# Performance work log

Hardware: AMD Instinct MI355X
Metric: run time of the kernel (lower is better)

Reference implementation:

```python
import jax, jax.numpy as jnp
import numpy as np

H, W = 32, 56
CK, CV = 64, 512
N = 16 * H * W  # long + work memory fully populated: 16 frames of H*W entries
TOP_K = 30


def setup_inputs() -> dict:
    key = jax.random.key(0)
    k1, k2, k3, k4, k5 = jax.random.split(key, 5)
    return {
        "q_key": jax.random.normal(k1, (1, CK, H, W), dtype=jnp.float32),
        "q_selection": jax.random.uniform(k2, (1, CK, H, W), dtype=jnp.float32),
        "mem_key": jax.random.normal(k3, (1, CK, N), dtype=jnp.float32),
        "mem_shrinkage": jax.random.uniform(k4, (1, N, 1), dtype=jnp.float32),
        "mem_value": jax.random.normal(k5, (2, CV, N), dtype=jnp.float32),
    }


def reference(q_key, q_selection, mem_key, mem_shrinkage, mem_value):
    b, ck, h, w = q_key.shape
    hw = h * w
    qk = q_key.reshape(1, ck, hw)          # [1, CK, HW]
    qs = q_selection.reshape(1, ck, hw)    # [1, CK, HW]

    mk = jnp.swapaxes(mem_key, 1, 2)       # [1, N, CK]
    # negative weighted squared L2 distance via matmul algebra
    a_sq = jnp.matmul(mk * mk, qs)                    # [1, N, HW]
    two_ab = 2.0 * jnp.matmul(mk, qk * qs)            # [1, N, HW]
    b_sq = jnp.sum(qs * qk * qk, axis=1, keepdims=True)  # [1, 1, HW]
    sim = (-a_sq + two_ab - b_sq) * mem_shrinkage / jnp.sqrt(jnp.float32(ck))  # [1, N, HW]

    # topk over the memory axis (dim=1), softmax over selected entries, scatter back
    simT = jnp.swapaxes(sim, 1, 2)                    # [1, HW, N]
    vals, idx = jax.lax.top_k(simT, TOP_K)            # [1, HW, K]
    x_exp = jnp.exp(vals)
    x_exp = x_exp / jnp.sum(x_exp, axis=-1, keepdims=True)
    i0 = jnp.arange(1)[:, None, None]
    i1 = jnp.arange(hw)[None, :, None]
    affT = jnp.zeros_like(simT).at[i0, i1, idx].set(x_exp)  # [1, HW, N]
    affinity = jnp.swapaxes(affT, 1, 2)               # [1, N, HW]

    out = jnp.matmul(mem_value, affinity)             # [2, CV, HW] (batch-broadcast)
    return out.reshape(2, CV, h, w)
```

## Files before the change

### kernel.cpp

```cpp
#include <hip/hip_runtime.h>
#include <math.h>

#define HW      1792
#define NMEM    28672
#define NCHUNK  3584
#define TOPK    30
#define CTARGET 64
#define BINS    4096
#define VCACHE  3072
#define SIMB    448
#define WPS     7

typedef __attribute__((ext_vector_type(8))) short bf16x8;
typedef __attribute__((ext_vector_type(8))) unsigned short u16x8;
typedef __attribute__((ext_vector_type(4))) float f32x4;
typedef __attribute__((ext_vector_type(4))) _Float16 h4;

static __device__ __forceinline__ unsigned short f2bf(float v) {
  unsigned b = __float_as_uint(v);
  return (unsigned short)((b + 0x7FFFu + ((b >> 16) & 1u)) >> 16);
}
static __device__ __forceinline__ float bf2f(unsigned short h) {
  return __uint_as_float(((unsigned)h) << 16);
}
static __device__ __forceinline__ unsigned fkey(float v) {
  return __float_as_uint(-v) & 0x7FFFFFFFu;
}
static __device__ __forceinline__ void gl_lds16(const void* g, void* l) {
  __builtin_amdgcn_global_load_lds(
      (const __attribute__((address_space(1))) unsigned*)g,
      (__attribute__((address_space(3))) unsigned*)l, 16, 0, 0);
}

__global__ __launch_bounds__(256)
void k_prep_b(const float* __restrict__ mk, const float* __restrict__ shr_in,
              unsigned short* __restrict__ Bh,
              float* __restrict__ mkT, float* __restrict__ shr_s)
{
  const int n = blockIdx.x * 256 + threadIdx.x;
  shr_s[n] = shr_in[n] * 0.125f;
  for (int cb = 0; cb < 64; cb += 8) {
    u16x8 h1, h2;
    float vv[8];
    #pragma unroll
    for (int j = 0; j < 8; ++j) {
      float v = mk[(size_t)(cb + j) * NMEM + n];
      vv[j] = v;
      h1[j] = f2bf(v);
      h2[j] = f2bf(v * v);
    }
    const int s = cb >> 3;
    *reinterpret_cast<u16x8*>(&Bh[((size_t)s * NMEM + n) * 8])       = h1;
    *reinterpret_cast<u16x8*>(&Bh[((size_t)(s + 8) * NMEM + n) * 8]) = h2;
    *reinterpret_cast<float4*>(&mkT[(size_t)n * 64 + cb])     = make_float4(vv[0], vv[1], vv[2], vv[3]);
    *reinterpret_cast<float4*>(&mkT[(size_t)n * 64 + cb + 4]) = make_float4(vv[4], vv[5], vv[6], vv[7]);
  }
}

__global__ __launch_bounds__(256)
void k_prep_u(const float* __restrict__ q_key, const float* __restrict__ q_sel,
              unsigned short* __restrict__ Uh, unsigned short* __restrict__ Ul,
              float* __restrict__ bsq)
{
  const int p = blockIdx.x * 256 + threadIdx.x;
  float bs = 0.f;
  for (int cb = 0; cb < 64; cb += 8) {
    u16x8 h1, l1, h2, l2;
    #pragma unroll
    for (int j = 0; j < 8; ++j) {
      int c = cb + j;
      float k = q_key[(size_t)c * HW + p];
      float s = q_sel[(size_t)c * HW + p];
      float u = 2.f * k * s;
      float w = -s;
      bs = fmaf(s * k, k, bs);
      unsigned short h = f2bf(u); h1[j] = h; l1[j] = f2bf(u - bf2f(h));
      unsigned short g = f2bf(w); h2[j] = g; l2[j] = f2bf(w - bf2f(g));
    }
    const int s = cb >> 3;
    *reinterpret_cast<u16x8*>(&Uh[((size_t)s * HW + p) * 8])       = h1;
    *reinterpret_cast<u16x8*>(&Ul[((size_t)s * HW + p) * 8])       = l1;
    *reinterpret_cast<u16x8*>(&Uh[((size_t)(s + 8) * HW + p) * 8]) = h2;
    *reinterpret_cast<u16x8*>(&Ul[((size_t)(s + 8) * HW + p) * 8]) = l2;
  }
  bsq[p] = bs;
}

__global__ __launch_bounds__(256, 2)
void k_sim(const unsigned short* __restrict__ Uh, const unsigned short* __restrict__ Ul,
           const unsigned short* __restrict__ Bh,
           const float* __restrict__ bsq, const float* __restrict__ shr_s,
           float* __restrict__ pmax)
{
  __shared__ char smem[65536] __attribute__((aligned(16)));
  const int tid = threadIdx.x;
  const int wid = tid >> 6, lane = tid & 63;
  const int lr = lane & 15, lg = lane >> 4;
  const int pb = blockIdx.x % 14, st = blockIdx.x / 14;
  const int pw = pb * 128 + wid * 32;
  const int w0 = st * WPS;

  bf16x8 a0h[4], a0l[4], a1h[4], a1l[4];
  #pragma unroll
  for (int t = 0; t < 4; ++t) {
    const size_t e0 = ((size_t)(t * 4 + lg) * HW + pw + lr) * 8;
    const size_t e1 = e0 + 16 * 8;
    a0h[t] = *reinterpret_cast<const bf16x8*>(&Uh[e0]);
    a0l[t] = *reinterpret_cast<const bf16x8*>(&Ul[e0]);
    a1h[t] = *reinterpret_cast<const bf16x8*>(&Uh[e1]);
    a1l[t] = *reinterpret_cast<const bf16x8*>(&Ul[e1]);
  }
  float bq[2][4];
  #pragma unroll
  for (int pt = 0; pt < 2; ++pt)
    #pragma unroll
    for (int r = 0; r < 4; ++r) bq[pt][r] = bsq[pw + pt * 16 + 4 * lg + r];

  auto stage = [&](int buf, int i) {
    const int n0 = (w0 + i) * 128;
    #pragma unroll
    for (int j = 0; j < 8; ++j) {
      const int idx = j * 256 + tid;
      const int s = idx >> 7, rr = idx & 127;
      gl_lds16((const char*)Bh + ((size_t)s * NMEM + n0 + rr) * 16,
               smem + buf * 32768 + idx * 16);
    }
  };

  stage(0, 0);
  int buf = 0;
  for (int i = 0; i < WPS; ++i) {
    __syncthreads();
    if (i + 1 < WPS) stage(buf ^ 1, i + 1);

    f32x4 acc[2][8];
    #pragma unroll
    for (int a = 0; a < 2; ++a)
      #pragma unroll
      for (int b = 0; b < 8; ++b) acc[a][b] = (f32x4){0.f, 0.f, 0.f, 0.f};

    const short* lb = (const short*)(smem + buf * 32768);
    #pragma unroll
    for (int t = 0; t < 4; ++t) {
      #pragma unroll
      for (int nt = 0; nt < 8; ++nt) {
        bf16x8 bh = *reinterpret_cast<const bf16x8*>(
            &lb[((t * 4 + lg) * 128 + nt * 16 + lr) * 8]);
        acc[0][nt] = __builtin_amdgcn_mfma_f32_16x16x32_bf16(a0h[t], bh, acc[0][nt], 0, 0, 0);
        acc[0][nt] = __builtin_amdgcn_mfma_f32_16x16x32_bf16(a0l[t], bh, acc[0][nt], 0, 0, 0);
        acc[1][nt] = __builtin_amdgcn_mfma_f32_16x16x32_bf16(a1h[t], bh, acc[1][nt], 0, 0, 0);
        acc[1][nt] = __builtin_amdgcn_mfma_f32_16x16x32_bf16(a1l[t], bh, acc[1][nt], 0, 0, 0);
      }
    }

    const int wgl = w0 + i;
    const int n0 = wgl * 128;
    float shv[8];
    #pragma unroll
    for (int nt = 0; nt < 8; ++nt) shv[nt] = shr_s[n0 + nt * 16 + lr];
    #pragma unroll
    for (int pt = 0; pt < 2; ++pt) {
      #pragma unroll
      for (int r = 0; r < 4; ++r) {
        float mx = -INFINITY;
        #pragma unroll
        for (int nt = 0; nt < 8; ++nt)
          mx = fmaxf(mx, (acc[pt][nt][r] - bq[pt][r]) * shv[nt]);
        pmax[(size_t)(pw + pt * 16 + 4 * lg + r) * NCHUNK + wgl * 16 + lr] = mx;
      }
    }
    buf ^= 1;
  }
}

__global__ __launch_bounds__(256)
void k_transpose_h(const float* __restrict__ mv, _Float16* __restrict__ mvT)
{
  __shared__ float t[64][65];
  const int n0 = blockIdx.x * 64, ch0 = blockIdx.y * 64;
  const int tid = threadIdx.x;
  for (int i = tid; i < 64 * 16; i += 256) {
    int r = i >> 4, c4 = (i & 15) << 2;
    float4 v = *reinterpret_cast<const float4*>(&mv[(size_t)(ch0 + r) * NMEM + n0 + c4]);
    t[r][c4] = v.x; t[r][c4 + 1] = v.y; t[r][c4 + 2] = v.z; t[r][c4 + 3] = v.w;
  }
  __syncthreads();
  for (int i = tid; i < 64 * 16; i += 256) {
    int r = i >> 4, c4 = (i & 15) << 2;
    h4 hv = {(_Float16)t[c4][r], (_Float16)t[c4 + 1][r],
             (_Float16)t[c4 + 2][r], (_Float16)t[c4 + 3][r]};
    *reinterpret_cast<h4*>(&mvT[(size_t)(n0 + r) * 1024 + ch0 + c4]) = hv;
  }
}

__device__ __forceinline__ void find_cross(int* hist, int* lsum, int* wsum,
                                           int tid, int target, int* sB, int* sNA)
{
  const int base = tid * (BINS / 256);
  int ls = 0;
  #pragma unroll
  for (int k = 0; k < BINS / 256; ++k) ls += hist[base + k];
  lsum[tid] = ls;
  __syncthreads();
  int lane = tid & 63, wv = tid >> 6;
  int v = ls;
  #pragma unroll
  for (int off = 1; off < 64; off <<= 1) {
    int t = __shfl_up(v, off);
    if (lane >= off) v += t;
  }
  if (lane == 63) wsum[wv] = v;
  __syncthreads();
  int wo = 0;
  for (int k = 0; k < wv; ++k) wo += wsum[k];
  int run = wo + v - ls;
  #pragma unroll 1
  for (int k = 0; k < BINS / 256; ++k) {
    int h = hist[base + k];
    if (run < target && run + h >= target) { *sB = base + k; *sNA = run; }
    run += h;
  }
  __syncthreads();
}

__global__ __launch_bounds__(256)
void k_select(const float* __restrict__ pmax, const float* __restrict__ mkT,
              const float* __restrict__ q_key, const float* __restrict__ q_sel,
              const float* __restrict__ shr_s,
              float* __restrict__ wgt, int* __restrict__ widx)
{
  __shared__ int            hist[BINS];
  __shared__ float          sqk[64], sqs[64];
  __shared__ unsigned short chl[NCHUNK];
  __shared__ float          vcache[VCACHE];
  __shared__ unsigned       au[96];
  __shared__ int            ai[96];
  __shared__ unsigned       bu[1024];
  __shared__ int            bi[1024];
  __shared__ float          fv[32];
  __shared__ int            fi[32];
  __shared__ float          ew[32];
  __shared__ int            lsum[256], wsum[4];
  __shared__ int            sB, sNA, cA, cB, sSC;
  __shared__ float          sSum;

  const int pix = blockIdx.x;
  const int tid = threadIdx.x;

  if (tid < 64) {
    sqk[tid] = q_key[(size_t)tid * HW + pix];
    sqs[tid] = q_sel[(size_t)tid * HW + pix];
  }
  for (int i = tid; i < BINS; i += 256) hist[i] = 0;
  if (tid == 0) { sSC = 0; cA = 0; cB = 0; }
  __syncthreads();

  float m[NCHUNK / 256];
  const float* pm = pmax + (size_t)pix * NCHUNK;
  #pragma unroll
  for (int j = 0; j < NCHUNK / 256; ++j) m[j] = pm[tid + 256 * j];
  #pragma unroll
  for (int j = 0; j < NCHUNK / 256; ++j) atomicAdd(&hist[fkey(m[j]) >> 19], 1);
  __syncthreads();
  find_cross(hist, lsum, wsum, tid, CTARGET, &sB, &sNA);
  {
    const int B = sB;
    #pragma unroll
    for (int j = 0; j < NCHUNK / 256; ++j)
      if ((int)(fkey(m[j]) >> 19) <= B) {
        int k = atomicAdd(&sSC, 1);
        chl[k] = (unsigned short)(tid + 256 * j);
      }
  }
  __syncthreads();
  const int SC = sSC, NC = SC * 8;
  for (int i = tid; i < BINS; i += 256) hist[i] = 0;
  __syncthreads();

  const float4* sqk4 = reinterpret_cast<const float4*>(sqk);
  const float4* sqs4 = reinterpret_cast<const float4*>(sqs);

  for (int c = tid; c < NC; c += 256) {
    const int cc = chl[c >> 3];
    const int n = ((cc >> 4) << 7) + (cc & 15) + ((c & 7) << 4);
    const float4* mr = reinterpret_cast<const float4*>(mkT + (size_t)n * 64);
    float s = 0.f;
    #pragma unroll
    for (int j = 0; j < 16; ++j) {
      float4 q = mr[j], k4 = sqk4[j], s4 = sqs4[j];
      float d0 = q.x - k4.x, d1 = q.y - k4.y, d2 = q.z - k4.z, d3 = q.w - k4.w;
      s = fmaf(s4.x * d0, d0, s); s = fmaf(s4.y * d1, d1, s);
      s = fmaf(s4.z * d2, d2, s); s = fmaf(s4.w * d3, d3, s);
    }
    float v = -s * shr_s[n];
    if (c < VCACHE) vcache[c] = v;
    atomicAdd(&hist[fkey(v) >> 19], 1);
  }
  __syncthreads();
  find_cross(hist, lsum, wsum, tid, TOPK, &sB, &sNA);

  {
    const int B2 = sB;
    for (int c = tid; c < NC; c += 256) {
      const int cc = chl[c >> 3];
      const int n = ((cc >> 4) << 7) + (cc & 15) + ((c & 7) << 4);
      float v;
      if (c < VCACHE) v = vcache[c];
      else {
        const float4* mr = reinterpret_cast<const float4*>(mkT + (size_t)n * 64);
        float s = 0.f;
        #pragma unroll
        for (int j = 0; j < 16; ++j) {
          float4 q = mr[j], k4 = sqk4[j], s4 = sqs4[j];
          float d0 = q.x - k4.x, d1 = q.y - k4.y, d2 = q.z - k4.z, d3 = q.w - k4.w;
          s = fmaf(s4.x * d0, d0, s); s = fmaf(s4.y * d1, d1, s);
          s = fmaf(s4.z * d2, d2, s); s = fmaf(s4.w * d3, d3, s);
        }
        v = -s * shr_s[n];
      }
      unsigned u = fkey(v);
      int bin = (int)(u >> 19);
      if (bin < B2)       { int k = atomicAdd(&cA, 1); au[k] = u; ai[k] = n; }
      else if (bin == B2) { int k = atomicAdd(&cB, 1); if (k < 1024) { bu[k] = u; bi[k] = n; } }
    }
  }
  __syncthreads();
  {
    const int nAv = cA, mm = (cB < 1024 ? cB : 1024), need = TOPK - nAv;
    for (int t = tid; t < mm; t += 256) {
      unsigned u = bu[t]; int id = bi[t];
      int r = 0;
      for (int k2 = 0; k2 < mm; ++k2) {
        unsigned uk = bu[k2];
        r += (uk < u) || (uk == u && bi[k2] < id);
      }
      if (r < need) { au[nAv + r] = u; ai[nAv + r] = id; }
    }
  }
  __syncthreads();

  if (tid < TOPK) {
    unsigned u = au[tid]; int id = ai[tid];
    int r = 0;
    for (int k2 = 0; k2 < TOPK; ++k2) {
      unsigned uk = au[k2];
      r += (uk < u) || (uk == u && ai[k2] < id);
    }
    fv[r] = -__uint_as_float(u); fi[r] = id;
  }
  __syncthreads();
  if (tid < 32) {
    float e = (tid < TOPK) ? expf(fv[tid]) : 0.f;
    if (tid < TOPK) ew[tid] = e;
    float ss = e;
    #pragma unroll
    for (int off = 16; off > 0; off >>= 1) ss += __shfl_down(ss, off);
    if (tid == 0) sSum = ss;
  }
  __syncthreads();
  if (tid < TOPK) {
    wgt [(size_t)pix * 32 + tid] = ew[tid] / sSum;
    widx[(size_t)pix * 32 + tid] = fi[tid];
  }
}

__global__ __launch_bounds__(256)
void k_gather_h(const _Float16* __restrict__ mvT, const float* __restrict__ wgt,
                const int* __restrict__ widx, float* __restrict__ out)
{
  __shared__ float sw[8][TOPK];
  __shared__ int   si[8][TOPK];
  __shared__ float sbuf[256][9];
  const int p0 = blockIdx.x * 8, chg = blockIdx.y * 256;
  const int tid = threadIdx.x;

  for (int i = tid; i < 8 * TOPK; i += 256) {
    int q = i / TOPK, k = i - q * TOPK;
    sw[q][k] = wgt [(size_t)(p0 + q) * 32 + k];
    si[q][k] = widx[(size_t)(p0 + q) * 32 + k];
  }
  __syncthreads();

  const int ch = chg + tid;
  #pragma unroll 2
  for (int q = 0; q < 8; ++q) {
    float a = 0.f;
    #pragma unroll
    for (int k = 0; k < TOPK; ++k)
      a = fmaf(sw[q][k], (float)mvT[(size_t)si[q][k] * 1024 + ch], a);
    sbuf[tid][q] = a;
  }
  __syncthreads();

  for (int i = tid; i < 256 * 8; i += 256) {
    int cl = i >> 3, q = i & 7;
    out[(size_t)(chg + cl) * HW + p0 + q] = sbuf[cl][q];
  }
}

__global__ __launch_bounds__(256)
void k_gather_f(const float* __restrict__ src, const float* __restrict__ wgt,
                const int* __restrict__ widx, float* __restrict__ out,
                long n_stride, long ch_stride)
{
  __shared__ float sw[8][TOPK];
  __shared__ int   si[8][TOPK];
  __shared__ float sbuf[256][9];
  const int p0 = blockIdx.x * 8, chg = blockIdx.y * 256;
  const int tid = threadIdx.x;

  for (int i = tid; i < 8 * TOPK; i += 256) {
    int q = i / TOPK, k = i - q * TOPK;
    sw[q][k] = wgt [(size_t)(p0 + q) * 32 + k];
    si[q][k] = widx[(size_t)(p0 + q) * 32 + k];
  }
  __syncthreads();

  const int ch = chg + tid;
  #pragma unroll 2
  for (int q = 0; q < 8; ++q) {
    float a = 0.f;
    #pragma unroll
    for (int k = 0; k < TOPK; ++k)
      a = fmaf(sw[q][k], src[(size_t)si[q][k] * n_stride + (size_t)ch * ch_stride], a);
    sbuf[tid][q] = a;
  }
  __syncthreads();

  for (int i = tid; i < 256 * 8; i += 256) {
    int cl = i >> 3, q = i & 7;
    out[(size_t)(chg + cl) * HW + p0 + q] = sbuf[cl][q];
  }
}

extern "C" void kernel_launch(void* const* d_in, const int* in_sizes, int n_in,
                              void* d_out, int out_size, void* d_ws, size_t ws_size,
                              hipStream_t stream)
{
  (void)in_sizes; (void)n_in; (void)out_size;
  const float* q_key     = (const float*)d_in[0];
  const float* q_sel     = (const float*)d_in[1];
  const float* mem_key   = (const float*)d_in[2];
  const float* mem_shr   = (const float*)d_in[3];
  const float* mem_value = (const float*)d_in[4];
  float* out = (float*)d_out;

  char* ws = (char*)d_ws;
  size_t off = 0;
  auto alloc = [&](size_t b) { size_t c = off; off = (off + b + 255) & ~(size_t)255; return c; };
  size_t o_w   = alloc((size_t)HW * 32 * 4);
  size_t o_wi  = alloc((size_t)HW * 32 * 4);
  size_t o_pr  = off;
  size_t o_bh  = alloc((size_t)NMEM * 128 * 2);
  size_t o_uh  = alloc((size_t)HW * 128 * 2);
  size_t o_ul  = alloc((size_t)HW * 128 * 2);
  size_t o_bsq = alloc((size_t)HW * 4);
  size_t o_shr = alloc((size_t)NMEM * 4);
  size_t o_mkT = alloc((size_t)NMEM * 64 * 4);
  size_t o_pm  = alloc((size_t)HW * NCHUNK * 4);
  size_t o_end = off;

  float*          wg   = (float*)(ws + o_w);
  int*            wi   = (int*)  (ws + o_wi);
  unsigned short* Bh   = (unsigned short*)(ws + o_bh);
  unsigned short* Uh   = (unsigned short*)(ws + o_uh);
  unsigned short* Ul   = (unsigned short*)(ws + o_ul);
  float*          bsq  = (float*)(ws + o_bsq);
  float*          shr  = (float*)(ws + o_shr);
  float*          mkT  = (float*)(ws + o_mkT);
  float*          pmx  = (float*)(ws + o_pm);

  const size_t mvh_sz = (size_t)NMEM * 1024 * 2;

  k_prep_b<<<NMEM / 256, 256, 0, stream>>>(mem_key, mem_shr, Bh, mkT, shr);
  k_prep_u<<<HW / 256, 256, 0, stream>>>(q_key, q_sel, Uh, Ul, bsq);
  k_sim<<<SIMB, 256, 0, stream>>>(Uh, Ul, Bh, bsq, shr, pmx);

  if (ws_size >= o_end + mvh_sz) {
    _Float16* mvT = (_Float16*)(ws + o_end);
    k_transpose_h<<<dim3(NMEM / 64, 16), 256, 0, stream>>>(mem_value, mvT);
    k_select<<<HW, 256, 0, stream>>>(pmx, mkT, q_key, q_sel, shr, wg, wi);
    k_gather_h<<<dim3(HW / 8, 4), 256, 0, stream>>>(mvT, wg, wi, out);
  } else {
    k_select<<<HW, 256, 0, stream>>>(pmx, mkT, q_key, q_sel, shr, wg, wi);
    if (ws_size >= o_pr + mvh_sz) {
      _Float16* mvT = (_Float16*)(ws + o_pr);
      k_transpose_h<<<dim3(NMEM / 64, 16), 256, 0, stream>>>(mem_value, mvT);
      k_gather_h<<<dim3(HW / 8, 4), 256, 0, stream>>>(mvT, wg, wi, out);
    } else {
      k_gather_f<<<dim3(HW / 8, 4), 256, 0, stream>>>(
          mem_value, wg, wi, out, 1, NMEM);
    }
  }
}
```

Measured before the change: 172.1 us.

## Fuse value transpose into top-k selection kernel and shrink shared memory

```diff
diff --git a/kernel.cpp b/kernel.cpp
--- a/kernel.cpp
+++ b/kernel.cpp
@@ -6,8 +6,10 @@
 #define NCHUNK  3584
 #define TOPK    30
 #define CTARGET 64
-#define BINS    4096
-#define VCACHE  3072
+#define BINS    2048
+#define BSHIFT  20
+#define VCACHE  2048
+#define BCAP    768
 #define SIMB    448
 #define WPS     7
 
@@ -173,6 +175,211 @@
   }
 }
 
+struct SelS {
+  int            hist[BINS];
+  unsigned short chl[NCHUNK];
+  float          vcache[VCACHE];
+  float          sqk[64], sqs[64];
+  unsigned       au[64];
+  int            ai[64];
+  unsigned       bu[BCAP];
+  int            bi[BCAP];
+  float          fv[32];
+  int            fi[32];
+  float          ew[32];
+  int            lsum[256];
+  int            wsum[4];
+  int            sB, sNA, cA, cB, sSC;
+  float          sSum;
+};
+union SMemU {
+  SelS  sel;
+  float tt[64][65];
+};
+
+__device__ __forceinline__ void find_cross(SelS& s, int tid, int target)
+{
+  const int base = tid * (BINS / 256);
+  int ls = 0;
+  #pragma unroll
+  for (int k = 0; k < BINS / 256; ++k) ls += s.hist[base + k];
+  s.lsum[tid] = ls;
+  __syncthreads();
+  int lane = tid & 63, wv = tid >> 6;
+  int v = ls;
+  #pragma unroll
+  for (int off = 1; off < 64; off <<= 1) {
+    int t = __shfl_up(v, off);
+    if (lane >= off) v += t;
+  }
+  if (lane == 63) s.wsum[wv] = v;
+  __syncthreads();
+  int wo = 0;
+  for (int k = 0; k < wv; ++k) wo += s.wsum[k];
+  int run = wo + v - ls;
+  #pragma unroll 1
+  for (int k = 0; k < BINS / 256; ++k) {
+    int h = s.hist[base + k];
+    if (run < target && run + h >= target) { s.sB = base + k; s.sNA = run; }
+    run += h;
+  }
+  __syncthreads();
+}
+
+__global__ __launch_bounds__(256, 4)
+void k_selT(const float* __restrict__ pmax, const float* __restrict__ mkT,
+            const float* __restrict__ q_key, const float* __restrict__ q_sel,
+            const float* __restrict__ shr_s,
+            float* __restrict__ wgt, int* __restrict__ widx,
+            const float* __restrict__ mv, _Float16* __restrict__ mvT)
+{
+  __shared__ SMemU sm;
+  const int tid = threadIdx.x;
+
+  int pix = -1, tb = -1;
+  if (gridDim.x > HW) {
+    const int g = blockIdx.x / 5, r = blockIdx.x % 5;
+    if (r == 0) pix = g; else tb = g * 4 + (r - 1);
+  } else {
+    pix = blockIdx.x;
+  }
+
+  if (tb >= 0) {
+    const int n0 = (tb % 448) * 64, ch0 = (tb / 448) * 64;
+    for (int i = tid; i < 64 * 16; i += 256) {
+      int r = i >> 4, c4 = (i & 15) << 2;
+      float4 v = *reinterpret_cast<const float4*>(&mv[(size_t)(ch0 + r) * NMEM + n0 + c4]);
+      sm.tt[r][c4] = v.x; sm.tt[r][c4 + 1] = v.y;
+      sm.tt[r][c4 + 2] = v.z; sm.tt[r][c4 + 3] = v.w;
+    }
+    __syncthreads();
+    for (int i = tid; i < 64 * 16; i += 256) {
+      int r = i >> 4, c4 = (i & 15) << 2;
+      h4 hv = {(_Float16)sm.tt[c4][r], (_Float16)sm.tt[c4 + 1][r],
+               (_Float16)sm.tt[c4 + 2][r], (_Float16)sm.tt[c4 + 3][r]};
+      *reinterpret_cast<h4*>(&mvT[(size_t)(n0 + r) * 1024 + ch0 + c4]) = hv;
+    }
+    return;
+  }
+
+  SelS& s = sm.sel;
+  if (tid < 64) {
+    s.sqk[tid] = q_key[(size_t)tid * HW + pix];
+    s.sqs[tid] = q_sel[(size_t)tid * HW + pix];
+  }
+  for (int i = tid; i < BINS; i += 256) s.hist[i] = 0;
+  if (tid == 0) { s.sSC = 0; s.cA = 0; s.cB = 0; }
+  __syncthreads();
+
+  float m[NCHUNK / 256];
+  const float* pm = pmax + (size_t)pix * NCHUNK;
+  #pragma unroll
+  for (int j = 0; j < NCHUNK / 256; ++j) m[j] = pm[tid + 256 * j];
+  #pragma unroll
+  for (int j = 0; j < NCHUNK / 256; ++j) atomicAdd(&s.hist[fkey(m[j]) >> BSHIFT], 1);
+  __syncthreads();
+  find_cross(s, tid, CTARGET);
+  {
+    const int B = s.sB;
+    #pragma unroll
+    for (int j = 0; j < NCHUNK / 256; ++j)
+      if ((int)(fkey(m[j]) >> BSHIFT) <= B) {
+        int k = atomicAdd(&s.sSC, 1);
+        s.chl[k] = (unsigned short)(tid + 256 * j);
+      }
+  }
+  __syncthreads();
+  const int NC = s.sSC * 8;
+  for (int i = tid; i < BINS; i += 256) s.hist[i] = 0;
+  __syncthreads();
+
+  const float4* sqk4 = reinterpret_cast<const float4*>(s.sqk);
+  const float4* sqs4 = reinterpret_cast<const float4*>(s.sqs);
+
+  for (int c = tid; c < NC; c += 256) {
+    const int cc = s.chl[c >> 3];
+    const int n = ((cc >> 4) << 7) + (cc & 15) + ((c & 7) << 4);
+    const float4* mr = reinterpret_cast<const float4*>(mkT + (size_t)n * 64);
+    float sv = 0.f;
+    #pragma unroll
+    for (int j = 0; j < 16; ++j) {
+      float4 q = mr[j], k4 = sqk4[j], s4 = sqs4[j];
+      float d0 = q.x - k4.x, d1 = q.y - k4.y, d2 = q.z - k4.z, d3 = q.w - k4.w;
+      sv = fmaf(s4.x * d0, d0, sv); sv = fmaf(s4.y * d1, d1, sv);
+      sv = fmaf(s4.z * d2, d2, sv); sv = fmaf(s4.w * d3, d3, sv);
+    }
+    float v = -sv * shr_s[n];
+    if (c < VCACHE) s.vcache[c] = v;
+    atomicAdd(&s.hist[fkey(v) >> BSHIFT], 1);
+  }
+  __syncthreads();
+  find_cross(s, tid, TOPK);
+
+  {
+    const int B2 = s.sB;
+    for (int c = tid; c < NC; c += 256) {
+      const int cc = s.chl[c >> 3];
+      const int n = ((cc >> 4) << 7) + (cc & 15) + ((c & 7) << 4);
+      float v;
+      if (c < VCACHE) v = s.vcache[c];
+      else {
+        const float4* mr = reinterpret_cast<const float4*>(mkT + (size_t)n * 64);
+        float sv = 0.f;
+        #pragma unroll
+        for (int j = 0; j < 16; ++j) {
+          float4 q = mr[j], k4 = sqk4[j], s4 = sqs4[j];
+          float d0 = q.x - k4.x, d1 = q.y - k4.y, d2 = q.z - k4.z, d3 = q.w - k4.w;
+          sv = fmaf(s4.x * d0, d0, sv); sv = fmaf(s4.y * d1, d1, sv);
+          sv = fmaf(s4.z * d2, d2, sv); sv = fmaf(s4.w * d3, d3, sv);
+        }
+        v = -sv * shr_s[n];
+      }
+      unsigned u = fkey(v);
+      int bin = (int)(u >> BSHIFT);
+      if (bin < B2)       { int k = atomicAdd(&s.cA, 1); s.au[k] = u; s.ai[k] = n; }
+      else if (bin == B2) { int k = atomicAdd(&s.cB, 1); if (k < BCAP) { s.bu[k] = u; s.bi[k] = n; } }
+    }
+  }
+  __syncthreads();
+  {
+    const int nAv = s.cA, mm = (s.cB < BCAP ? s.cB : BCAP), need = TOPK - nAv;
+    for (int t = tid; t < mm; t += 256) {
+      unsigned u = s.bu[t]; int id = s.bi[t];
+      int r = 0;
+      for (int k2 = 0; k2 < mm; ++k2) {
+        unsigned uk = s.bu[k2];
+        r += (uk < u) || (uk == u && s.bi[k2] < id);
+      }
+      if (r < need) { s.au[nAv + r] = u; s.ai[nAv + r] = id; }
+    }
+  }
+  __syncthreads();
+
+  if (tid < TOPK) {
+    unsigned u = s.au[tid]; int id = s.ai[tid];
+    int r = 0;
+    for (int k2 = 0; k2 < TOPK; ++k2) {
+      unsigned uk = s.au[k2];
+      r += (uk < u) || (uk == u && s.ai[k2] < id);
+    }
+    s.fv[r] = -__uint_as_float(u); s.fi[r] = id;
+  }
+  __syncthreads();
+  if (tid < 32) {
+    float e = (tid < TOPK) ? expf(s.fv[tid]) : 0.f;
+    if (tid < TOPK) s.ew[tid] = e;
+    float ss = e;
+    #pragma unroll
+    for (int off = 16; off > 0; off >>= 1) ss += __shfl_down(ss, off);
+    if (tid == 0) s.sSum = ss;
+  }
+  __syncthreads();
+  if (tid < TOPK) {
+    wgt [(size_t)pix * 32 + tid] = s.ew[tid] / s.sSum;
+    widx[(size_t)pix * 32 + tid] = s.fi[tid];
+  }
+}
+
 __global__ __launch_bounds__(256)
 void k_transpose_h(const float* __restrict__ mv, _Float16* __restrict__ mvT)
 {
@@ -190,177 +397,6 @@
     h4 hv = {(_Float16)t[c4][r], (_Float16)t[c4 + 1][r],
              (_Float16)t[c4 + 2][r], (_Float16)t[c4 + 3][r]};
     *reinterpret_cast<h4*>(&mvT[(size_t)(n0 + r) * 1024 + ch0 + c4]) = hv;
-  }
-}
-
-__device__ __forceinline__ void find_cross(int* hist, int* lsum, int* wsum,
-                                           int tid, int target, int* sB, int* sNA)
-{
-  const int base = tid * (BINS / 256);
-  int ls = 0;
-  #pragma unroll
-  for (int k = 0; k < BINS / 256; ++k) ls += hist[base + k];
-  lsum[tid] = ls;
-  __syncthreads();
-  int lane = tid & 63, wv = tid >> 6;
-  int v = ls;
-  #pragma unroll
-  for (int off = 1; off < 64; off <<= 1) {
-    int t = __shfl_up(v, off);
-    if (lane >= off) v += t;
-  }
-  if (lane == 63) wsum[wv] = v;
-  __syncthreads();
-  int wo = 0;
-  for (int k = 0; k < wv; ++k) wo += wsum[k];
-  int run = wo + v - ls;
-  #pragma unroll 1
-  for (int k = 0; k < BINS / 256; ++k) {
-    int h = hist[base + k];
-    if (run < target && run + h >= target) { *sB = base + k; *sNA = run; }
-    run += h;
-  }
-  __syncthreads();
-}
-
-__global__ __launch_bounds__(256)
-void k_select(const float* __restrict__ pmax, const float* __restrict__ mkT,
-              const float* __restrict__ q_key, const float* __restrict__ q_sel,
-              const float* __restrict__ shr_s,
-              float* __restrict__ wgt, int* __restrict__ widx)
-{
-  __shared__ int            hist[BINS];
-  __shared__ float          sqk[64], sqs[64];
-  __shared__ unsigned short chl[NCHUNK];
-  __shared__ float          vcache[VCACHE];
-  __shared__ unsigned       au[96];
-  __shared__ int            ai[96];
-  __shared__ unsigned       bu[1024];
-  __shared__ int            bi[1024];
-  __shared__ float          fv[32];
-  __shared__ int            fi[32];
-  __shared__ float          ew[32];
-  __shared__ int            lsum[256], wsum[4];
-  __shared__ int            sB, sNA, cA, cB, sSC;
-  __shared__ float          sSum;
-
-  const int pix = blockIdx.x;
-  const int tid = threadIdx.x;
-
-  if (tid < 64) {
-    sqk[tid] = q_key[(size_t)tid * HW + pix];
-    sqs[tid] = q_sel[(size_t)tid * HW + pix];
-  }
-  for (int i = tid; i < BINS; i += 256) hist[i] = 0;
-  if (tid == 0) { sSC = 0; cA = 0; cB = 0; }
-  __syncthreads();
-
-  float m[NCHUNK / 256];
-  const float* pm = pmax + (size_t)pix * NCHUNK;
-  #pragma unroll
-  for (int j = 0; j < NCHUNK / 256; ++j) m[j] = pm[tid + 256 * j];
-  #pragma unroll
-  for (int j = 0; j < NCHUNK / 256; ++j) atomicAdd(&hist[fkey(m[j]) >> 19], 1);
-  __syncthreads();
-  find_cross(hist, lsum, wsum, tid, CTARGET, &sB, &sNA);
-  {
-    const int B = sB;
-    #pragma unroll
-    for (int j = 0; j < NCHUNK / 256; ++j)
-      if ((int)(fkey(m[j]) >> 19) <= B) {
-        int k = atomicAdd(&sSC, 1);
-        chl[k] = (unsigned short)(tid + 256 * j);
-      }
-  }
-  __syncthreads();
-  const int SC = sSC, NC = SC * 8;
-  for (int i = tid; i < BINS; i += 256) hist[i] = 0;
-  __syncthreads();
-
-  const float4* sqk4 = reinterpret_cast<const float4*>(sqk);
-  const float4* sqs4 = reinterpret_cast<const float4*>(sqs);
-
-  for (int c = tid; c < NC; c += 256) {
-    const int cc = chl[c >> 3];
-    const int n = ((cc >> 4) << 7) + (cc & 15) + ((c & 7) << 4);
-    const float4* mr = reinterpret_cast<const float4*>(mkT + (size_t)n * 64);
-    float s = 0.f;
-    #pragma unroll
-    for (int j = 0; j < 16; ++j) {
-      float4 q = mr[j], k4 = sqk4[j], s4 = sqs4[j];
-      float d0 = q.x - k4.x, d1 = q.y - k4.y, d2 = q.z - k4.z, d3 = q.w - k4.w;
-      s = fmaf(s4.x * d0, d0, s); s = fmaf(s4.y * d1, d1, s);
-      s = fmaf(s4.z * d2, d2, s); s = fmaf(s4.w * d3, d3, s);
-    }
-    float v = -s * shr_s[n];
-    if (c < VCACHE) vcache[c] = v;
-    atomicAdd(&hist[fkey(v) >> 19], 1);
-  }
-  __syncthreads();
-  find_cross(hist, lsum, wsum, tid, TOPK, &sB, &sNA);
-
-  {
-    const int B2 = sB;
-    for (int c = tid; c < NC; c += 256) {
-      const int cc = chl[c >> 3];
-      const int n = ((cc >> 4) << 7) + (cc & 15) + ((c & 7) << 4);
-      float v;
-      if (c < VCACHE) v = vcache[c];
-      else {
-        const float4* mr = reinterpret_cast<const float4*>(mkT + (size_t)n * 64);
-        float s = 0.f;
-        #pragma unroll
-        for (int j = 0; j < 16; ++j) {
-          float4 q = mr[j], k4 = sqk4[j], s4 = sqs4[j];
-          float d0 = q.x - k4.x, d1 = q.y - k4.y, d2 = q.z - k4.z, d3 = q.w - k4.w;
-          s = fmaf(s4.x * d0, d0, s); s = fmaf(s4.y * d1, d1, s);
-          s = fmaf(s4.z * d2, d2, s); s = fmaf(s4.w * d3, d3, s);
-        }
-        v = -s * shr_s[n];
-      }
-      unsigned u = fkey(v);
-      int bin = (int)(u >> 19);
-      if (bin < B2)       { int k = atomicAdd(&cA, 1); au[k] = u; ai[k] = n; }
-      else if (bin == B2) { int k = atomicAdd(&cB, 1); if (k < 1024) { bu[k] = u; bi[k] = n; } }
-    }
-  }
-  __syncthreads();
-  {
-    const int nAv = cA, mm = (cB < 1024 ? cB : 1024), need = TOPK - nAv;
-    for (int t = tid; t < mm; t += 256) {
-      unsigned u = bu[t]; int id = bi[t];
-      int r = 0;
-      for (int k2 = 0; k2 < mm; ++k2) {
-        unsigned uk = bu[k2];
-        r += (uk < u) || (uk == u && bi[k2] < id);
-      }
-      if (r < need) { au[nAv + r] = u; ai[nAv + r] = id; }
-    }
-  }
-  __syncthreads();
-
-  if (tid < TOPK) {
-    unsigned u = au[tid]; int id = ai[tid];
-    int r = 0;
-    for (int k2 = 0; k2 < TOPK; ++k2) {
-      unsigned uk = au[k2];
-      r += (uk < u) || (uk == u && ai[k2] < id);
-    }
-    fv[r] = -__uint_as_float(u); fi[r] = id;
-  }
-  __syncthreads();
-  if (tid < 32) {
-    float e = (tid < TOPK) ? expf(fv[tid]) : 0.f;
-    if (tid < TOPK) ew[tid] = e;
-    float ss = e;
-    #pragma unroll
-    for (int off = 16; off > 0; off >>= 1) ss += __shfl_down(ss, off);
-    if (tid == 0) sSum = ss;
-  }
-  __syncthreads();
-  if (tid < TOPK) {
-    wgt [(size_t)pix * 32 + tid] = ew[tid] / sSum;
-    widx[(size_t)pix * 32 + tid] = fi[tid];
   }
 }
 
@@ -478,11 +514,12 @@
 
   if (ws_size >= o_end + mvh_sz) {
     _Float16* mvT = (_Float16*)(ws + o_end);
-    k_transpose_h<<<dim3(NMEM / 64, 16), 256, 0, stream>>>(mem_value, mvT);
-    k_select<<<HW, 256, 0, stream>>>(pmx, mkT, q_key, q_sel, shr, wg, wi);
+    k_selT<<<HW * 5, 256, 0, stream>>>(pmx, mkT, q_key, q_sel, shr,
+                                       wg, wi, mem_value, mvT);
     k_gather_h<<<dim3(HW / 8, 4), 256, 0, stream>>>(mvT, wg, wi, out);
   } else {
-    k_select<<<HW, 256, 0, stream>>>(pmx, mkT, q_key, q_sel, shr, wg, wi);
+    k_selT<<<HW, 256, 0, stream>>>(pmx, mkT, q_key, q_sel, shr,
+                                   wg, wi, mem_value, nullptr);
     if (ws_size >= o_pr + mvh_sz) {
       _Float16* mvT = (_Float16*)(ws + o_pr);
       k_transpose_h<<<dim3(NMEM / 64, 16), 256, 0, stream>>>(mem_value, mvT);
```

After: 143.5 us. 1.2x faster.

## Rewrite top-k select as one wavefront per pixel with two-level radix and argmax

Applied to the files above, without the earlier changes.

```diff
diff --git a/kernel.cpp b/kernel.cpp
--- a/kernel.cpp
+++ b/kernel.cpp
@@ -6,8 +6,7 @@
 #define NCHUNK  3584
 #define TOPK    30
 #define CTARGET 64
-#define BINS    4096
-#define VCACHE  3072
+#define SCAP    80
 #define SIMB    448
 #define WPS     7
 
@@ -31,6 +30,8 @@
       (const __attribute__((address_space(1))) unsigned*)g,
       (__attribute__((address_space(3))) unsigned*)l, 16, 0, 0);
 }
+#define WSYNC() do { asm volatile("s_waitcnt lgkmcnt(0)" ::: "memory"); \
+                     __builtin_amdgcn_wave_barrier(); } while (0)
 
 __global__ __launch_bounds__(256)
 void k_prep_b(const float* __restrict__ mk, const float* __restrict__ shr_in,
@@ -173,6 +174,160 @@
   }
 }
 
+__device__ __forceinline__ void wave_cross(const int* h, int lane, int target,
+                                           int& B, int& nA)
+{
+  int hv[16]; int ls = 0;
+  #pragma unroll
+  for (int k = 0; k < 16; ++k) { hv[k] = h[(k << 6) + lane]; ls += hv[k]; }
+  int sc = ls;
+  #pragma unroll
+  for (int off = 1; off < 64; off <<= 1) {
+    int t = __shfl_up(sc, off);
+    if (lane >= off) sc += t;
+  }
+  int run = sc - ls;
+  int myB = -1, mynA = 0;
+  #pragma unroll
+  for (int k = 0; k < 16; ++k) {
+    if (run < target && run + hv[k] >= target) { myB = lane * 16 + k; mynA = run; }
+    run += hv[k];
+  }
+  unsigned long long ball = __ballot(myB >= 0);
+  int src = __ffsll((long long)ball) - 1;
+  B = __shfl(myB, src); nA = __shfl(mynA, src);
+}
+
+__global__ __launch_bounds__(256, 2)
+void k_select(const float* __restrict__ pmax, const float* __restrict__ mkT,
+              const float* __restrict__ q_key, const float* __restrict__ q_sel,
+              const float* __restrict__ shr_s,
+              float* __restrict__ wgt, int* __restrict__ widx)
+{
+  __shared__ int                hist[4][1024];
+  __shared__ unsigned long long pk[4][640];
+  __shared__ short              slist[4][SCAP];
+  __shared__ float              sqk[4][64], sqs[4][64];
+
+  const int w = threadIdx.x >> 6, lane = threadIdx.x & 63;
+  const int pix = blockIdx.x * 4 + w;
+  int* h = hist[w];
+  unsigned long long* p = pk[w];
+  short* sl = slist[w];
+
+  auto ph = [](int b) { return ((b & 15) << 6) | (b >> 4); };
+
+  sqk[w][lane] = q_key[(size_t)lane * HW + pix];
+  sqs[w][lane] = q_sel[(size_t)lane * HW + pix];
+
+  float m[56];
+  const float* pm = pmax + (size_t)pix * NCHUNK;
+  #pragma unroll
+  for (int j = 0; j < 56; ++j) m[j] = pm[lane + 64 * j];
+
+  #pragma unroll
+  for (int k = 0; k < 16; ++k) h[lane + 64 * k] = 0;
+  WSYNC();
+  #pragma unroll
+  for (int j = 0; j < 56; ++j) atomicAdd(&h[ph(fkey(m[j]) >> 21)], 1);
+  WSYNC();
+  int B1, nA1;
+  wave_cross(h, lane, CTARGET, B1, nA1);
+
+  #pragma unroll
+  for (int k = 0; k < 16; ++k) h[lane + 64 * k] = 0;
+  WSYNC();
+  #pragma unroll
+  for (int j = 0; j < 56; ++j) {
+    unsigned u = fkey(m[j]);
+    if ((int)(u >> 21) == B1) atomicAdd(&h[ph((u >> 11) & 1023)], 1);
+  }
+  WSYNC();
+  int Bs1, nAs1;
+  wave_cross(h, lane, CTARGET - nA1, Bs1, nAs1);
+
+  int nsurv = 0;
+  #pragma unroll
+  for (int j = 0; j < 56; ++j) {
+    unsigned u = fkey(m[j]);
+    int bin = (int)(u >> 21);
+    bool keep = (bin < B1) || (bin == B1 && (int)((u >> 11) & 1023) <= Bs1);
+    unsigned long long ball = __ballot(keep);
+    if (keep) {
+      int pos = nsurv + __popcll(ball & ((1ull << lane) - 1ull));
+      if (pos < SCAP) sl[pos] = (short)(lane + 64 * j);
+    }
+    nsurv += __popcll(ball);
+  }
+  nsurv = (nsurv < SCAP) ? nsurv : SCAP;
+  const int NC = nsurv * 8;
+
+  #pragma unroll
+  for (int t = 0; t < 10; ++t) p[lane + (t << 6)] = 0ull;
+  WSYNC();
+  const float4* k4p = reinterpret_cast<const float4*>(sqk[w]);
+  const float4* s4p = reinterpret_cast<const float4*>(sqs[w]);
+  for (int c = lane; c < NC; c += 64) {
+    const int cc = sl[c >> 3];
+    const int n = ((cc >> 4) << 7) + (cc & 15) + ((c & 7) << 4);
+    const float4* mr = reinterpret_cast<const float4*>(mkT + (size_t)n * 64);
+    float a0 = 0.f, a1 = 0.f, a2 = 0.f, a3 = 0.f;
+    #pragma unroll
+    for (int j = 0; j < 16; j += 4) {
+      #pragma unroll
+      for (int jj = 0; jj < 4; ++jj) {
+        float4 q = mr[j + jj], kk = k4p[j + jj], ss = s4p[j + jj];
+        float d0 = q.x - kk.x, d1 = q.y - kk.y, d2 = q.z - kk.z, d3 = q.w - kk.w;
+        float pj = fmaf(ss.x * d0, d0,
+                   fmaf(ss.y * d1, d1,
+                   fmaf(ss.z * d2, d2, ss.w * d3 * d3)));
+        if (jj == 0) a0 += pj; else if (jj == 1) a1 += pj;
+        else if (jj == 2) a2 += pj; else a3 += pj;
+      }
+    }
+    float v = -((a0 + a1) + (a2 + a3)) * shr_s[n];
+    p[c] = ((unsigned long long)(0x7FFFFFFFu - fkey(v)) << 32) |
+           (unsigned long long)(0xFFFFFFFFu - (unsigned)n);
+  }
+  WSYNC();
+
+  unsigned long long bk = 0ull; int bp = -1;
+  #pragma unroll
+  for (int t = 0; t < 10; ++t) {
+    unsigned long long v = p[lane + (t << 6)];
+    if (v > bk) { bk = v; bp = lane + (t << 6); }
+  }
+  float esum = 0.f, myv = 0.f;
+  int myn = 0;
+  for (int r = 0; r < TOPK; ++r) {
+    unsigned long long gk = bk; int gp = bp;
+    #pragma unroll
+    for (int off = 1; off < 64; off <<= 1) {
+      unsigned long long ok = __shfl_xor(gk, off);
+      int op = __shfl_xor(gp, off);
+      if (ok > gk) { gk = ok; gp = op; }
+    }
+    float v = -__uint_as_float(0x7FFFFFFFu - (unsigned)(gk >> 32));
+    int n = (int)(0xFFFFFFFFu - (unsigned)(gk & 0xFFFFFFFFu));
+    esum += expf(v);
+    if (lane == r) { myv = v; myn = n; }
+    if (lane == (gp & 63)) {
+      p[gp] = 0ull;
+      asm volatile("s_waitcnt lgkmcnt(0)" ::: "memory");
+      bk = 0ull; bp = -1;
+      #pragma unroll
+      for (int t = 0; t < 10; ++t) {
+        unsigned long long vv = p[lane + (t << 6)];
+        if (vv > bk) { bk = vv; bp = lane + (t << 6); }
+      }
+    }
+  }
+  if (lane < TOPK) {
+    wgt [(size_t)pix * 32 + lane] = expf(myv) / esum;
+    widx[(size_t)pix * 32 + lane] = myn;
+  }
+}
+
 __global__ __launch_bounds__(256)
 void k_transpose_h(const float* __restrict__ mv, _Float16* __restrict__ mvT)
 {
@@ -190,177 +345,6 @@
     h4 hv = {(_Float16)t[c4][r], (_Float16)t[c4 + 1][r],
              (_Float16)t[c4 + 2][r], (_Float16)t[c4 + 3][r]};
     *reinterpret_cast<h4*>(&mvT[(size_t)(n0 + r) * 1024 + ch0 + c4]) = hv;
-  }
-}
-
-__device__ __forceinline__ void find_cross(int* hist, int* lsum, int* wsum,
-                                           int tid, int target, int* sB, int* sNA)
-{
-  const int base = tid * (BINS / 256);
-  int ls = 0;
-  #pragma unroll
-  for (int k = 0; k < BINS / 256; ++k) ls += hist[base + k];
-  lsum[tid] = ls;
-  __syncthreads();
-  int lane = tid & 63, wv = tid >> 6;
-  int v = ls;
-  #pragma unroll
-  for (int off = 1; off < 64; off <<= 1) {
-    int t = __shfl_up(v, off);
-    if (lane >= off) v += t;
-  }
-  if (lane == 63) wsum[wv] = v;
-  __syncthreads();
-  int wo = 0;
-  for (int k = 0; k < wv; ++k) wo += wsum[k];
-  int run = wo + v - ls;
-  #pragma unroll 1
-  for (int k = 0; k < BINS / 256; ++k) {
-    int h = hist[base + k];
-    if (run < target && run + h >= target) { *sB = base + k; *sNA = run; }
-    run += h;
-  }
-  __syncthreads();
-}
-
-__global__ __launch_bounds__(256)
-void k_select(const float* __restrict__ pmax, const float* __restrict__ mkT,
-              const float* __restrict__ q_key, const float* __restrict__ q_sel,
-              const float* __restrict__ shr_s,
-              float* __restrict__ wgt, int* __restrict__ widx)
-{
-  __shared__ int            hist[BINS];
-  __shared__ float          sqk[64], sqs[64];
-  __shared__ unsigned short chl[NCHUNK];
-  __shared__ float          vcache[VCACHE];
-  __shared__ unsigned       au[96];
-  __shared__ int            ai[96];
-  __shared__ unsigned       bu[1024];
-  __shared__ int            bi[1024];
-  __shared__ float          fv[32];
-  __shared__ int            fi[32];
-  __shared__ float          ew[32];
-  __shared__ int            lsum[256], wsum[4];
-  __shared__ int            sB, sNA, cA, cB, sSC;
-  __shared__ float          sSum;
-
-  const int pix = blockIdx.x;
-  const int tid = threadIdx.x;
-
-  if (tid < 64) {
-    sqk[tid] = q_key[(size_t)tid * HW + pix];
-    sqs[tid] = q_sel[(size_t)tid * HW + pix];
-  }
-  for (int i = tid; i < BINS; i += 256) hist[i] = 0;
-  if (tid == 0) { sSC = 0; cA = 0; cB = 0; }
-  __syncthreads();
-
-  float m[NCHUNK / 256];
-  const float* pm = pmax + (size_t)pix * NCHUNK;
-  #pragma unroll
-  for (int j = 0; j < NCHUNK / 256; ++j) m[j] = pm[tid + 256 * j];
-  #pragma unroll
-  for (int j = 0; j < NCHUNK / 256; ++j) atomicAdd(&hist[fkey(m[j]) >> 19], 1);
-  __syncthreads();
-  find_cross(hist, lsum, wsum, tid, CTARGET, &sB, &sNA);
-  {
-    const int B = sB;
-    #pragma unroll
-    for (int j = 0; j < NCHUNK / 256; ++j)
-      if ((int)(fkey(m[j]) >> 19) <= B) {
-        int k = atomicAdd(&sSC, 1);
-        chl[k] = (unsigned short)(tid + 256 * j);
-      }
-  }
-  __syncthreads();
-  const int SC = sSC, NC = SC * 8;
-  for (int i = tid; i < BINS; i += 256) hist[i] = 0;
-  __syncthreads();
-
-  const float4* sqk4 = reinterpret_cast<const float4*>(sqk);
-  const float4* sqs4 = reinterpret_cast<const float4*>(sqs);
-
-  for (int c = tid; c < NC; c += 256) {
-    const int cc = chl[c >> 3];
-    const int n = ((cc >> 4) << 7) + (cc & 15) + ((c & 7) << 4);
-    const float4* mr = reinterpret_cast<const float4*>(mkT + (size_t)n * 64);
-    float s = 0.f;
-    #pragma unroll
-    for (int j = 0; j < 16; ++j) {
-      float4 q = mr[j], k4 = sqk4[j], s4 = sqs4[j];
-      float d0 = q.x - k4.x, d1 = q.y - k4.y, d2 = q.z - k4.z, d3 = q.w - k4.w;
-      s = fmaf(s4.x * d0, d0, s); s = fmaf(s4.y * d1, d1, s);
-      s = fmaf(s4.z * d2, d2, s); s = fmaf(s4.w * d3, d3, s);
-    }
-    float v = -s * shr_s[n];
-    if (c < VCACHE) vcache[c] = v;
-    atomicAdd(&hist[fkey(v) >> 19], 1);
-  }
-  __syncthreads();
-  find_cross(hist, lsum, wsum, tid, TOPK, &sB, &sNA);
-
-  {
-    const int B2 = sB;
-    for (int c = tid; c < NC; c += 256) {
-      const int cc = chl[c >> 3];
-      const int n = ((cc >> 4) << 7) + (cc & 15) + ((c & 7) << 4);
-      float v;
-      if (c < VCACHE) v = vcache[c];
-      else {
-        const float4* mr = reinterpret_cast<const float4*>(mkT + (size_t)n * 64);
-        float s = 0.f;
-        #pragma unroll
-        for (int j = 0; j < 16; ++j) {
-          float4 q = mr[j], k4 = sqk4[j], s4 = sqs4[j];
-          float d0 = q.x - k4.x, d1 = q.y - k4.y, d2 = q.z - k4.z, d3 = q.w - k4.w;
-          s = fmaf(s4.x * d0, d0, s); s = fmaf(s4.y * d1, d1, s);
-          s = fmaf(s4.z * d2, d2, s); s = fmaf(s4.w * d3, d3, s);
-        }
-        v = -s * shr_s[n];
-      }
-      unsigned u = fkey(v);
-      int bin = (int)(u >> 19);
-      if (bin < B2)       { int k = atomicAdd(&cA, 1); au[k] = u; ai[k] = n; }
-      else if (bin == B2) { int k = atomicAdd(&cB, 1); if (k < 1024) { bu[k] = u; bi[k] = n; } }
-    }
-  }
-  __syncthreads();
-  {
-    const int nAv = cA, mm = (cB < 1024 ? cB : 1024), need = TOPK - nAv;
-    for (int t = tid; t < mm; t += 256) {
-      unsigned u = bu[t]; int id = bi[t];
-      int r = 0;
-      for (int k2 = 0; k2 < mm; ++k2) {
-        unsigned uk = bu[k2];
-        r += (uk < u) || (uk == u && bi[k2] < id);
-      }
-      if (r < need) { au[nAv + r] = u; ai[nAv + r] = id; }
-    }
-  }
-  __syncthreads();
-
-  if (tid < TOPK) {
-    unsigned u = au[tid]; int id = ai[tid];
-    int r = 0;
-    for (int k2 = 0; k2 < TOPK; ++k2) {
-      unsigned uk = au[k2];
-      r += (uk < u) || (uk == u && ai[k2] < id);
-    }
-    fv[r] = -__uint_as_float(u); fi[r] = id;
-  }
-  __syncthreads();
-  if (tid < 32) {
-    float e = (tid < TOPK) ? expf(fv[tid]) : 0.f;
-    if (tid < TOPK) ew[tid] = e;
-    float ss = e;
-    #pragma unroll
-    for (int off = 16; off > 0; off >>= 1) ss += __shfl_down(ss, off);
-    if (tid == 0) sSum = ss;
-  }
-  __syncthreads();
-  if (tid < TOPK) {
-    wgt [(size_t)pix * 32 + tid] = ew[tid] / sSum;
-    widx[(size_t)pix * 32 + tid] = fi[tid];
   }
 }
 
@@ -475,21 +459,18 @@
   k_prep_b<<<NMEM / 256, 256, 0, stream>>>(mem_key, mem_shr, Bh, mkT, shr);
   k_prep_u<<<HW / 256, 256, 0, stream>>>(q_key, q_sel, Uh, Ul, bsq);
   k_sim<<<SIMB, 256, 0, stream>>>(Uh, Ul, Bh, bsq, shr, pmx);
+  k_select<<<HW / 4, 256, 0, stream>>>(pmx, mkT, q_key, q_sel, shr, wg, wi);
 
   if (ws_size >= o_end + mvh_sz) {
     _Float16* mvT = (_Float16*)(ws + o_end);
     k_transpose_h<<<dim3(NMEM / 64, 16), 256, 0, stream>>>(mem_value, mvT);
-    k_select<<<HW, 256, 0, stream>>>(pmx, mkT, q_key, q_sel, shr, wg, wi);
+    k_gather_h<<<dim3(HW / 8, 4), 256, 0, stream>>>(mvT, wg, wi, out);
+  } else if (ws_size >= o_pr + mvh_sz) {
+    _Float16* mvT = (_Float16*)(ws + o_pr);
+    k_transpose_h<<<dim3(NMEM / 64, 16), 256, 0, stream>>>(mem_value, mvT);
     k_gather_h<<<dim3(HW / 8, 4), 256, 0, stream>>>(mvT, wg, wi, out);
   } else {
-    k_select<<<HW, 256, 0, stream>>>(pmx, mkT, q_key, q_sel, shr, wg, wi);
-    if (ws_size >= o_pr + mvh_sz) {
-      _Float16* mvT = (_Float16*)(ws + o_pr);
-      k_transpose_h<<<dim3(NMEM / 64, 16), 256, 0, stream>>>(mem_value, mvT);
-      k_gather_h<<<dim3(HW / 8, 4), 256, 0, stream>>>(mvT, wg, wi, out);
-    } else {
-      k_gather_f<<<dim3(HW / 8, 4), 256, 0, stream>>>(
-          mem_value, wg, wi, out, 1, NMEM);
-    }
-  }
-}
+    k_gather_f<<<dim3(HW / 8, 4), 256, 0, stream>>>(
+        mem_value, wg, wi, out, 1, NMEM);
+  }
+}
```

New measurement: 169.7 us. Within noise of the previous version (-1.4%).
